# Kernel optimization log

Hardware: AMD Instinct MI355X
Metric: run time of the kernel (lower is better)

Reference implementation:

```python
import jax, jax.numpy as jnp
import numpy as np

B, NT, NC, NN = 2, 64, 1024, 1024
C, H = 1024, 16
HD = C // H
N = NT + NC + NN
EPS = 1e-5
NEG = -1e30


def _ln(t, w, b):
    # LayerNorm over last dim (head_dim), torch eps=1e-5
    mu = jnp.mean(t, axis=-1, keepdims=True)
    var = jnp.mean(jnp.square(t - mu), axis=-1, keepdims=True)
    return (t - mu) * jax.lax.rsqrt(var + EPS) * w + b


def _rope(q, k, pos):
    # q,k: [B,H,S,HD]; pos: [B,S]; rotate-half RoPE, base 10000
    hd = q.shape[-1]
    half = hd // 2
    inv_freq = 1.0 / (10000.0 ** (jnp.arange(half, dtype=jnp.float32) / half))
    ang = pos.astype(jnp.float32)[:, None, :, None] * inv_freq  # [B,1,S,half]
    cos, sin = jnp.cos(ang), jnp.sin(ang)
    def rot(t):
        t1, t2 = t[..., :half], t[..., half:]
        return jnp.concatenate([t1 * cos - t2 * sin, t2 * cos + t1 * sin], axis=-1)
    return rot(q), rot(k)


def setup_inputs() -> dict:
    key = jax.random.key(0)
    ks = jax.random.split(key, 4)
    s = 0.02
    return {
        "x": jax.random.normal(ks[0], (B, N, C), jnp.float32),
        "position_ids": jnp.broadcast_to(jnp.arange(NC + NN, dtype=jnp.int32), (B, NC + NN)),
        "text_position_ids": jnp.broadcast_to(jnp.arange(NT, dtype=jnp.int32), (B, NT)),
        "attention_mask": jnp.tril(jnp.ones((N, N), dtype=bool)),
        "n_text": NT, "n_clean": NC, "n_noised": NN,
        "qkv_w": jax.random.normal(ks[1], (3, 3 * C, C), jnp.float32) * s,
        "qkv_b": jnp.zeros((3, 3 * C), jnp.float32),
        "qn_w": jnp.ones((3, HD), jnp.float32),
        "qn_b": jnp.zeros((3, HD), jnp.float32),
        "kn_w": jnp.ones((3, HD), jnp.float32),
        "kn_b": jnp.zeros((3, HD), jnp.float32),
        "proj_w": jax.random.normal(ks[2], (3, C, C), jnp.float32) * s,
        "proj_b": jnp.zeros((3, C), jnp.float32),
    }


def reference(x, position_ids, text_position_ids, attention_mask, n_text, n_clean, n_noised,
              qkv_w, qkv_b, qn_w, qn_b, kn_w, kn_b, proj_w, proj_b):
    Bx, Nx, Cx = x.shape
    hd = qn_w.shape[-1]
    nh = Cx // hd
    b0, b1 = n_text, n_text + n_clean
    segs = (x[:, :b0], x[:, b0:b1], x[:, b1:])  # text / clean / noised

    qs, kks, vvs = [], [], []
    for i, xs in enumerate(segs):
        S = xs.shape[1]
        qkv = jnp.einsum('bsc,oc->bso', xs, qkv_w[i]) + qkv_b[i]
        qkv = qkv.reshape(Bx, S, 3, nh, hd).transpose(2, 0, 3, 1, 4)  # [3,B,H,S,hd]
        q = _ln(qkv[0], qn_w[i], qn_b[i])
        k = _ln(qkv[1], kn_w[i], kn_b[i])
        qs.append(q); kks.append(k); vvs.append(qkv[2])

    img_q = jnp.concatenate([qs[1], qs[2]], axis=2)
    img_k = jnp.concatenate([kks[1], kks[2]], axis=2)
    img_q, img_k = _rope(img_q, img_k, position_ids)
    txt_q, txt_k = _rope(qs[0], kks[0], text_position_ids)

    q = jnp.concatenate([txt_q, img_q], axis=2)
    k = jnp.concatenate([txt_k, img_k], axis=2)
    v = jnp.concatenate(vvs, axis=2)

    scale = 1.0 / np.sqrt(hd).astype(np.float32)
    scores = jnp.einsum('bhqd,bhkd->bhqk', q, k) * scale
    scores = jnp.where(attention_mask, scores, NEG)
    attn = jax.nn.softmax(scores, axis=-1)
    out = jnp.einsum('bhqk,bhkd->bhqd', attn, v)
    out = out.transpose(0, 2, 1, 3).reshape(Bx, Nx, Cx)

    o_segs = (out[:, :b0], out[:, b0:b1], out[:, b1:])
    outs = [jnp.einsum('bsc,oc->bso', o_segs[i], proj_w[i]) + proj_b[i] for i in range(3)]
    return jnp.concatenate(outs, axis=1)
```

## Files before the change

kernel.cpp:

```cpp
#include <hip/hip_runtime.h>
#include <hip/hip_bf16.h>

#define BB   2
#define NT   64
#define NC   1024
#define NN   1024
#define NTOK (NT + NC + NN)
#define CC   1024
#define HH   16
#define HD   64
#define K3   (3 * CC)
#define EPSV 1e-5f

typedef __attribute__((ext_vector_type(8))) short short8;
typedef __attribute__((ext_vector_type(4))) float f32x4;

__device__ __forceinline__ short bf16raw(float x) {
    __hip_bfloat16 h = __float2bfloat16(x);
    return *(short*)&h;
}

#define GL_LDS(gptr, lptr) \
    __builtin_amdgcn_global_load_lds( \
        (const __attribute__((address_space(1))) void*)(gptr), \
        (__attribute__((address_space(3))) void*)(lptr), 16, 0, 0)

__global__ __launch_bounds__(256) void cast_bf16(const float* __restrict__ src,
                                                 __hip_bfloat16* __restrict__ dst, int n) {
    int i = blockIdx.x * 256 + threadIdx.x;
    int stride = gridDim.x * 256;
    for (; i < n; i += stride) dst[i] = __float2bfloat16(src[i]);
}

__global__ __launch_bounds__(256) void gemm_qkv(
    const __hip_bfloat16* __restrict__ A,
    const __hip_bfloat16* __restrict__ Wb,
    const float* __restrict__ biasb,
    const int* __restrict__ pos_ids,
    const int* __restrict__ tpos_ids,
    const float* __restrict__ qn_w, const float* __restrict__ qn_b,
    const float* __restrict__ kn_w, const float* __restrict__ kn_b,
    __hip_bfloat16* __restrict__ Q,
    __hip_bfloat16* __restrict__ Kg,
    __hip_bfloat16* __restrict__ Vt)
{
    __shared__ short buf[128 * 134];
    short* As = buf;
    short* Bs = buf + 4096;

    int tid = threadIdx.x;
    int lane = tid & 63, w = tid >> 6;
    int l15 = lane & 15, quad = lane >> 4;
    int wm = w >> 1, wn = w & 1;

    int y = blockIdx.y;
    int seg, tm;
    if (y < 16)      { seg = 1; tm = y * 128; }
    else if (y < 32) { seg = 2; tm = (y - 16) * 128; }
    else             { seg = 0; tm = 0; }
    int S = (seg == 0) ? 64 : 1024;
    int seg_start = (seg == 0) ? 0 : (seg == 1 ? NT : NT + NC);
    const short* W = (const short*)Wb + (size_t)seg * K3 * CC;
    const float* bias = biasb + (size_t)seg * K3;
    int tileN = blockIdx.x * 128;

    const short* aptr[2];
    const short* bptr[2];
#pragma unroll
    for (int j = 0; j < 2; ++j) {
        int c = j * 256 + tid;
        int row = c >> 2, u = c & 3;
        int ar = tm + row;
        int arow = (ar / S) * NTOK + seg_start + (ar % S);
        aptr[j] = (const short*)A + (size_t)arow * CC + u * 8;
        bptr[j] = W + (size_t)(tileN + row) * CC + u * 8;
    }

    f32x4 zero = {0.f, 0.f, 0.f, 0.f};
    f32x4 acc[4][4];
#pragma unroll
    for (int mb = 0; mb < 4; ++mb)
#pragma unroll
        for (int nb = 0; nb < 4; ++nb) acc[mb][nb] = zero;

    for (int k0 = 0; k0 < CC; k0 += 32) {
        __syncthreads();
#pragma unroll
        for (int j = 0; j < 2; ++j) {
            int c8 = (j * 256 + tid) * 8;
            GL_LDS(aptr[j] + k0, As + c8);
            GL_LDS(bptr[j] + k0, Bs + c8);
        }
        __syncthreads();

        short8 af[4], bf[4];
#pragma unroll
        for (int mb = 0; mb < 4; ++mb)
            af[mb] = *(const short8*)&As[((wm * 64 + mb * 16 + l15) * 4 + quad) * 8];
#pragma unroll
        for (int nb = 0; nb < 4; ++nb)
            bf[nb] = *(const short8*)&Bs[((wn * 64 + nb * 16 + l15) * 4 + quad) * 8];
#pragma unroll
        for (int mb = 0; mb < 4; ++mb)
#pragma unroll
            for (int nb = 0; nb < 4; ++nb)
                acc[mb][nb] = __builtin_amdgcn_mfma_f32_16x16x32_bf16(af[mb], bf[nb], acc[mb][nb], 0, 0, 0);
    }

    int sect = tileN >> 10;
    int head = ((tileN & 1023) >> 6) + wn;

    if (sect < 2) {
        const float* nw = (sect == 0 ? qn_w : kn_w) + seg * HD;
        const float* nbv = (sect == 0 ? qn_b : kn_b) + seg * HD;
        float lw[4], lb[4], bcol[4];
#pragma unroll
        for (int nb = 0; nb < 4; ++nb) {
            lw[nb] = nw[nb * 16 + l15];
            lb[nb] = nbv[nb * 16 + l15];
            bcol[nb] = bias[tileN + wn * 64 + nb * 16 + l15];
        }
        float invf0 = expf(-9.210340371976184f * (float)l15 * (1.0f / 32.0f));
        float invf1 = expf(-9.210340371976184f * (float)(16 + l15) * (1.0f / 32.0f));
        __hip_bfloat16* dst = (sect == 0) ? Q : Kg;
        float qscale = (sect == 0) ? 0.125f : 1.0f;

#pragma unroll
        for (int mb = 0; mb < 4; ++mb) {
#pragma unroll
            for (int r = 0; r < 4; ++r) {
                int ar = tm + wm * 64 + mb * 16 + quad * 4 + r;
                int bb = ar / S;
                int nloc = seg_start + (ar % S);
                float v[4];
#pragma unroll
                for (int nb = 0; nb < 4; ++nb) v[nb] = acc[mb][nb][r] + bcol[nb];

                float mu = v[0] + v[1] + v[2] + v[3];
#pragma unroll
                for (int off = 8; off >= 1; off >>= 1) mu += __shfl_xor(mu, off);
                mu *= (1.0f / 64.0f);
                float t[4];
                float var = 0.f;
#pragma unroll
                for (int nb = 0; nb < 4; ++nb) { t[nb] = v[nb] - mu; var += t[nb] * t[nb]; }
#pragma unroll
                for (int off = 8; off >= 1; off >>= 1) var += __shfl_xor(var, off);
                var *= (1.0f / 64.0f);
                float rstd = rsqrtf(var + EPSV);
#pragma unroll
                for (int nb = 0; nb < 4; ++nb) v[nb] = t[nb] * rstd * lw[nb] + lb[nb];

                int pos = (seg == 0) ? tpos_ids[bb * NT + nloc]
                                     : pos_ids[bb * (NC + NN) + (nloc - NT)];
                float s0, c0, s1, c1;
                sincosf((float)pos * invf0, &s0, &c0);
                sincosf((float)pos * invf1, &s1, &c1);
                float o0 = (v[0] * c0 - v[2] * s0) * qscale;
                float o1 = (v[1] * c1 - v[3] * s1) * qscale;
                float o2 = (v[2] * c0 + v[0] * s0) * qscale;
                float o3 = (v[3] * c1 + v[1] * s1) * qscale;

                short* dp = (short*)dst + ((size_t)(bb * HH + head) * NTOK + nloc) * HD;
                dp[0 * 16 + l15] = bf16raw(o0);
                dp[1 * 16 + l15] = bf16raw(o1);
                dp[2 * 16 + l15] = bf16raw(o2);
                dp[3 * 16 + l15] = bf16raw(o3);
            }
        }
    } else {
        __syncthreads();
        float bcol[4];
#pragma unroll
        for (int nb = 0; nb < 4; ++nb) bcol[nb] = bias[tileN + wn * 64 + nb * 16 + l15];
#pragma unroll
        for (int mb = 0; mb < 4; ++mb) {
#pragma unroll
            for (int r = 0; r < 4; ++r) {
                int tok = wm * 64 + mb * 16 + quad * 4 + r;
#pragma unroll
                for (int nb = 0; nb < 4; ++nb) {
                    int col = wn * 64 + nb * 16 + l15;
                    buf[col * 134 + tok] = bf16raw(acc[mb][nb][r] + bcol[nb]);
                }
            }
        }
        __syncthreads();
#pragma unroll
        for (int it = 0; it < 8; ++it) {
            int idx = it * 256 + tid;
            int row = idx >> 4;
            int tc = (idx & 15) * 8;
            int vcol = (tileN - 2048) + row;
            int h = vcol >> 6, d = vcol & 63;
            int ar = tm + tc;
            int bb = ar / S;
            int nloc = seg_start + (ar % S);
            short8 val = *(const short8*)&buf[row * 134 + tc];
            *(short8*)((short*)Vt + ((size_t)(bb * HH + h) * HD + d) * NTOK + nloc) = val;
        }
    }
}

__global__ __launch_bounds__(256) void gemm128(
    const __hip_bfloat16* __restrict__ A,
    const __hip_bfloat16* __restrict__ Wb,
    const float* __restrict__ biasb,
    float* __restrict__ Cout,
    int Kdim, int Nout)
{
    __shared__ short As[128 * 32];
    __shared__ short Bs[128 * 32];

    int tid = threadIdx.x;
    int lane = tid & 63, w = tid >> 6;
    int l15 = lane & 15, quad = lane >> 4;
    int wm = w >> 1, wn = w & 1;

    int y = blockIdx.y;
    int seg, tm;
    if (y < 16)      { seg = 1; tm = y * 128; }
    else if (y < 32) { seg = 2; tm = (y - 16) * 128; }
    else             { seg = 0; tm = 0; }
    int S = (seg == 0) ? 64 : 1024;
    int seg_start = (seg == 0) ? 0 : (seg == 1 ? NT : NT + NC);
    const short* W = (const short*)Wb + (size_t)seg * Nout * Kdim;
    const float* bias = biasb + (size_t)seg * Nout;
    int tileN = blockIdx.x * 128;

    const short* aptr[2];
    const short* bptr[2];
#pragma unroll
    for (int j = 0; j < 2; ++j) {
        int c = j * 256 + tid;
        int row = c >> 2, u = c & 3;
        int ar = tm + row;
        int arow = (ar / S) * NTOK + seg_start + (ar % S);
        aptr[j] = (const short*)A + (size_t)arow * Kdim + u * 8;
        bptr[j] = W + (size_t)(tileN + row) * Kdim + u * 8;
    }

    f32x4 zero = {0.f, 0.f, 0.f, 0.f};
    f32x4 acc[4][4];
#pragma unroll
    for (int mb = 0; mb < 4; ++mb)
#pragma unroll
        for (int nb = 0; nb < 4; ++nb) acc[mb][nb] = zero;

    for (int k0 = 0; k0 < Kdim; k0 += 32) {
        __syncthreads();
#pragma unroll
        for (int j = 0; j < 2; ++j) {
            int c8 = (j * 256 + tid) * 8;
            GL_LDS(aptr[j] + k0, As + c8);
            GL_LDS(bptr[j] + k0, Bs + c8);
        }
        __syncthreads();

        short8 af[4], bf[4];
#pragma unroll
        for (int mb = 0; mb < 4; ++mb)
            af[mb] = *(const short8*)&As[((wm * 64 + mb * 16 + l15) * 4 + quad) * 8];
#pragma unroll
        for (int nb = 0; nb < 4; ++nb)
            bf[nb] = *(const short8*)&Bs[((wn * 64 + nb * 16 + l15) * 4 + quad) * 8];
#pragma unroll
        for (int mb = 0; mb < 4; ++mb)
#pragma unroll
            for (int nb = 0; nb < 4; ++nb)
                acc[mb][nb] = __builtin_amdgcn_mfma_f32_16x16x32_bf16(af[mb], bf[nb], acc[mb][nb], 0, 0, 0);
    }

#pragma unroll
    for (int mb = 0; mb < 4; ++mb) {
#pragma unroll
        for (int r = 0; r < 4; ++r) {
            int ar = tm + wm * 64 + mb * 16 + quad * 4 + r;
            int crow = (ar / S) * NTOK + seg_start + (ar % S);
            float* cp = Cout + (size_t)crow * Nout + tileN;
#pragma unroll
            for (int nb = 0; nb < 4; ++nb) {
                int col = wn * 64 + nb * 16 + l15;
                cp[col] = acc[mb][nb][r] + bias[tileN + col];
            }
        }
    }
}

__global__ __launch_bounds__(256) void attn_mfma(
    const __hip_bfloat16* __restrict__ Q,
    const __hip_bfloat16* __restrict__ Kg,
    const __hip_bfloat16* __restrict__ Vt,
    __hip_bfloat16* __restrict__ O)
{
    __shared__ short Ks[64][72];
    __shared__ short Vs[64][72];
    __shared__ short Ps[4][16][72];

    int tid = threadIdx.x;
    int lane = tid & 63, w = tid >> 6;
    int quad = lane >> 4, l15 = lane & 15;
    int bh = blockIdx.y, b = bh >> 4, h = bh & 15;
    int q0 = (gridDim.x - 1 - blockIdx.x) * 64;
    size_t base = (size_t)bh * NTOK * HD;

    int qrow = q0 + w * 16 + l15;
    short8 qf0 = *(const short8*)((const short*)Q + base + (size_t)qrow * HD + quad * 8);
    short8 qf1 = *(const short8*)((const short*)Q + base + (size_t)qrow * HD + 32 + quad * 8);

    f32x4 zero = {0.f, 0.f, 0.f, 0.f};
    f32x4 oacc[4] = {zero, zero, zero, zero};
    float l[4] = {0.f, 0.f, 0.f, 0.f};

    int ntiles = q0 / 64 + 1;

    for (int t = 0; t < ntiles; ++t) {
        __syncthreads();
        for (int i = tid; i < 512; i += 256) {
            int r = i >> 3, c = (i & 7) * 8;
            *(short8*)&Ks[r][c] = *(const short8*)((const short*)Kg + base + (size_t)(t * 64 + r) * HD + c);
            *(short8*)&Vs[r][c] = *(const short8*)((const short*)Vt + base + (size_t)r * NTOK + t * 64 + c);
        }
        __syncthreads();

        f32x4 s[4];
#pragma unroll
        for (int kb = 0; kb < 4; ++kb) {
            short8 kf0 = *(const short8*)&Ks[kb * 16 + l15][quad * 8];
            short8 kf1 = *(const short8*)&Ks[kb * 16 + l15][32 + quad * 8];
            f32x4 z = zero;
            z = __builtin_amdgcn_mfma_f32_16x16x32_bf16(qf0, kf0, z, 0, 0, 0);
            z = __builtin_amdgcn_mfma_f32_16x16x32_bf16(qf1, kf1, z, 0, 0, 0);
            s[kb] = z;
        }

#pragma unroll
        for (int r = 0; r < 4; ++r) {
            int qg = q0 + w * 16 + quad * 4 + r;
#pragma unroll
            for (int kb = 0; kb < 4; ++kb) {
                int kgk = t * 64 + kb * 16 + l15;
                float p = (kgk <= qg) ? __expf(s[kb][r]) : 0.f;
                Ps[w][quad * 4 + r][kb * 16 + l15] = bf16raw(p);
                l[r] += p;
            }
        }

        __builtin_amdgcn_wave_barrier();

#pragma unroll
        for (int sl = 0; sl < 2; ++sl) {
            short8 pf = *(const short8*)&Ps[w][l15][sl * 32 + quad * 8];
#pragma unroll
            for (int db = 0; db < 4; ++db) {
                short8 vf = *(const short8*)&Vs[db * 16 + l15][sl * 32 + quad * 8];
                oacc[db] = __builtin_amdgcn_mfma_f32_16x16x32_bf16(pf, vf, oacc[db], 0, 0, 0);
            }
        }
    }

#pragma unroll
    for (int r = 0; r < 4; ++r) {
#pragma unroll
        for (int off = 8; off >= 1; off >>= 1) l[r] += __shfl_xor(l[r], off);
    }

#pragma unroll
    for (int r = 0; r < 4; ++r) {
        int qg = q0 + w * 16 + quad * 4 + r;
        float inv_l = 1.0f / l[r];
#pragma unroll
        for (int db = 0; db < 4; ++db) {
            O[(size_t)(b * NTOK + qg) * CC + h * HD + db * 16 + l15] =
                __float2bfloat16(oacc[db][r] * inv_l);
        }
    }
}

extern "C" void kernel_launch(void* const* d_in, const int* in_sizes, int n_in,
                              void* d_out, int out_size, void* d_ws, size_t ws_size,
                              hipStream_t stream) {
    const float* x      = (const float*)d_in[0];
    const int* pos_ids  = (const int*)d_in[1];
    const int* tpos_ids = (const int*)d_in[2];
    const float* qkv_w  = (const float*)d_in[7];
    const float* qkv_b  = (const float*)d_in[8];
    const float* qn_w   = (const float*)d_in[9];
    const float* qn_b   = (const float*)d_in[10];
    const float* kn_w   = (const float*)d_in[11];
    const float* kn_b   = (const float*)d_in[12];
    const float* proj_w = (const float*)d_in[13];
    const float* proj_b = (const float*)d_in[14];
    float* out = (float*)d_out;

    const size_t n_x    = (size_t)BB * NTOK * CC;
    const size_t n_qkvw = (size_t)3 * K3 * CC;
    const size_t n_prjw = (size_t)3 * CC * CC;

    __hip_bfloat16* x_bf    = (__hip_bfloat16*)d_ws;
    __hip_bfloat16* qkvw_bf = x_bf + n_x;
    __hip_bfloat16* prjw_bf = qkvw_bf + n_qkvw;
    __hip_bfloat16* Qbf  = prjw_bf + n_prjw;
    __hip_bfloat16* Kbf  = Qbf + n_x;
    __hip_bfloat16* Vtbf = Kbf + n_x;
    __hip_bfloat16* attn_bf = x_bf;

    cast_bf16<<<(int)((n_x + 255) / 256), 256, 0, stream>>>(x, x_bf, (int)n_x);
    cast_bf16<<<(int)((n_qkvw + 255) / 256), 256, 0, stream>>>(qkv_w, qkvw_bf, (int)n_qkvw);
    cast_bf16<<<(int)((n_prjw + 255) / 256), 256, 0, stream>>>(proj_w, prjw_bf, (int)n_prjw);

    gemm_qkv<<<dim3(K3 / 128, 33), 256, 0, stream>>>(
        x_bf, qkvw_bf, qkv_b, pos_ids, tpos_ids,
        qn_w, qn_b, kn_w, kn_b, Qbf, Kbf, Vtbf);

    attn_mfma<<<dim3(NTOK / 64, BB * HH), 256, 0, stream>>>(Qbf, Kbf, Vtbf, attn_bf);

    gemm128<<<dim3(CC / 128, 33), 256, 0, stream>>>(
        attn_bf, prjw_bf, proj_b, out, CC, CC);
}
```

Before: 319.8 us.

## Fuse casts, widen GEMM K-tiles with XOR swizzle, coalesce QK stores, enlarge attention tiles

Merges the three fp32-to-bf16 cast launches into one vectorized kernel. The QKV and projection GEMMs now use BK=64 tiles with an XOR-swizzled LDS layout to cut bank conflicts and halve the barrier count. Q/K epilogue outputs are staged through LDS so global writes become 16-byte rows. The projection GEMM moves to 64-row M tiles, doubling the block count for better occupancy. Attention loads 128-key tiles, and a wave skips compute when the whole tile lies past its causal limit, at the cost of extra LDS per block.

```diff
diff --git a/kernel.cpp b/kernel.cpp
--- a/kernel.cpp
+++ b/kernel.cpp
@@ -14,6 +14,7 @@
 
 typedef __attribute__((ext_vector_type(8))) short short8;
 typedef __attribute__((ext_vector_type(4))) float f32x4;
+typedef __attribute__((ext_vector_type(4))) float float4v;
 
 __device__ __forceinline__ short bf16raw(float x) {
     __hip_bfloat16 h = __float2bfloat16(x);
@@ -25,11 +26,24 @@
         (const __attribute__((address_space(1))) void*)(gptr), \
         (__attribute__((address_space(3))) void*)(lptr), 16, 0, 0)
 
-__global__ __launch_bounds__(256) void cast_bf16(const float* __restrict__ src,
-                                                 __hip_bfloat16* __restrict__ dst, int n) {
+__global__ __launch_bounds__(256) void cast_all(
+    const float* __restrict__ s0, const float* __restrict__ s1, const float* __restrict__ s2,
+    __hip_bfloat16* __restrict__ d0, __hip_bfloat16* __restrict__ d1, __hip_bfloat16* __restrict__ d2,
+    int n0, int n1, int n2)
+{
     int i = blockIdx.x * 256 + threadIdx.x;
     int stride = gridDim.x * 256;
-    for (; i < n; i += stride) dst[i] = __float2bfloat16(src[i]);
+    int ntot = n0 + n1 + n2;
+    for (; i < ntot; i += stride) {
+        const float* sp; short* dp; int j;
+        if (i < n0)            { sp = s0; dp = (short*)d0; j = i; }
+        else if (i < n0 + n1)  { sp = s1; dp = (short*)d1; j = i - n0; }
+        else                   { sp = s2; dp = (short*)d2; j = i - n0 - n1; }
+        float4v v = *(const float4v*)(sp + (size_t)j * 4);
+        short4 o;
+        o.x = bf16raw(v.x); o.y = bf16raw(v.y); o.z = bf16raw(v.z); o.w = bf16raw(v.w);
+        *(short4*)(dp + (size_t)j * 4) = o;
+    }
 }
 
 __global__ __launch_bounds__(256) void gemm_qkv(
@@ -46,12 +60,13 @@
 {
     __shared__ short buf[128 * 134];
     short* As = buf;
-    short* Bs = buf + 4096;
+    short* Bs = buf + 8192;
 
     int tid = threadIdx.x;
     int lane = tid & 63, w = tid >> 6;
     int l15 = lane & 15, quad = lane >> 4;
     int wm = w >> 1, wn = w & 1;
+    int r7 = l15 & 7;
 
     int y = blockIdx.y;
     int seg, tm;
@@ -64,12 +79,12 @@
     const float* bias = biasb + (size_t)seg * K3;
     int tileN = blockIdx.x * 128;
 
-    const short* aptr[2];
-    const short* bptr[2];
-#pragma unroll
-    for (int j = 0; j < 2; ++j) {
+    const short* aptr[4];
+    const short* bptr[4];
+#pragma unroll
+    for (int j = 0; j < 4; ++j) {
         int c = j * 256 + tid;
-        int row = c >> 2, u = c & 3;
+        int row = c >> 3, u = (c & 7) ^ (row & 7);
         int ar = tm + row;
         int arow = (ar / S) * NTOK + seg_start + (ar % S);
         aptr[j] = (const short*)A + (size_t)arow * CC + u * 8;
@@ -83,32 +98,36 @@
 #pragma unroll
         for (int nb = 0; nb < 4; ++nb) acc[mb][nb] = zero;
 
-    for (int k0 = 0; k0 < CC; k0 += 32) {
-        __syncthreads();
-#pragma unroll
-        for (int j = 0; j < 2; ++j) {
+    for (int k0 = 0; k0 < CC; k0 += 64) {
+        __syncthreads();
+#pragma unroll
+        for (int j = 0; j < 4; ++j) {
             int c8 = (j * 256 + tid) * 8;
             GL_LDS(aptr[j] + k0, As + c8);
             GL_LDS(bptr[j] + k0, Bs + c8);
         }
         __syncthreads();
 
-        short8 af[4], bf[4];
-#pragma unroll
-        for (int mb = 0; mb < 4; ++mb)
-            af[mb] = *(const short8*)&As[((wm * 64 + mb * 16 + l15) * 4 + quad) * 8];
-#pragma unroll
-        for (int nb = 0; nb < 4; ++nb)
-            bf[nb] = *(const short8*)&Bs[((wn * 64 + nb * 16 + l15) * 4 + quad) * 8];
-#pragma unroll
-        for (int mb = 0; mb < 4; ++mb)
+#pragma unroll
+        for (int s = 0; s < 2; ++s) {
+            int sx = ((s * 4 + quad) ^ r7) * 8;
+            short8 af[4], bf[4];
+#pragma unroll
+            for (int mb = 0; mb < 4; ++mb)
+                af[mb] = *(const short8*)&As[(wm * 64 + mb * 16 + l15) * 64 + sx];
 #pragma unroll
             for (int nb = 0; nb < 4; ++nb)
-                acc[mb][nb] = __builtin_amdgcn_mfma_f32_16x16x32_bf16(af[mb], bf[nb], acc[mb][nb], 0, 0, 0);
+                bf[nb] = *(const short8*)&Bs[(wn * 64 + nb * 16 + l15) * 64 + sx];
+#pragma unroll
+            for (int mb = 0; mb < 4; ++mb)
+#pragma unroll
+                for (int nb = 0; nb < 4; ++nb)
+                    acc[mb][nb] = __builtin_amdgcn_mfma_f32_16x16x32_bf16(af[mb], bf[nb], acc[mb][nb], 0, 0, 0);
+        }
     }
 
     int sect = tileN >> 10;
-    int head = ((tileN & 1023) >> 6) + wn;
+    __syncthreads();
 
     if (sect < 2) {
         const float* nw = (sect == 0 ? qn_w : kn_w) + seg * HD;
@@ -122,14 +141,14 @@
         }
         float invf0 = expf(-9.210340371976184f * (float)l15 * (1.0f / 32.0f));
         float invf1 = expf(-9.210340371976184f * (float)(16 + l15) * (1.0f / 32.0f));
-        __hip_bfloat16* dst = (sect == 0) ? Q : Kg;
         float qscale = (sect == 0) ? 0.125f : 1.0f;
 
 #pragma unroll
         for (int mb = 0; mb < 4; ++mb) {
 #pragma unroll
             for (int r = 0; r < 4; ++r) {
-                int ar = tm + wm * 64 + mb * 16 + quad * 4 + r;
+                int tok = wm * 64 + mb * 16 + quad * 4 + r;
+                int ar = tm + tok;
                 int bb = ar / S;
                 int nloc = seg_start + (ar % S);
                 float v[4];
@@ -156,20 +175,28 @@
                 float s0, c0, s1, c1;
                 sincosf((float)pos * invf0, &s0, &c0);
                 sincosf((float)pos * invf1, &s1, &c1);
-                float o0 = (v[0] * c0 - v[2] * s0) * qscale;
-                float o1 = (v[1] * c1 - v[3] * s1) * qscale;
-                float o2 = (v[2] * c0 + v[0] * s0) * qscale;
-                float o3 = (v[3] * c1 + v[1] * s1) * qscale;
-
-                short* dp = (short*)dst + ((size_t)(bb * HH + head) * NTOK + nloc) * HD;
-                dp[0 * 16 + l15] = bf16raw(o0);
-                dp[1 * 16 + l15] = bf16raw(o1);
-                dp[2 * 16 + l15] = bf16raw(o2);
-                dp[3 * 16 + l15] = bf16raw(o3);
-            }
+                short* bp = &buf[tok * 134 + wn * 64];
+                bp[0 * 16 + l15] = bf16raw((v[0] * c0 - v[2] * s0) * qscale);
+                bp[1 * 16 + l15] = bf16raw((v[1] * c1 - v[3] * s1) * qscale);
+                bp[2 * 16 + l15] = bf16raw((v[2] * c0 + v[0] * s0) * qscale);
+                bp[3 * 16 + l15] = bf16raw((v[3] * c1 + v[1] * s1) * qscale);
+            }
+        }
+        __syncthreads();
+        __hip_bfloat16* dst = (sect == 0) ? Q : Kg;
+        int head_base = (tileN & 1023) >> 6;
+#pragma unroll
+        for (int it = 0; it < 8; ++it) {
+            int idx = it * 256 + tid;
+            int tok = idx >> 4, cc = (idx & 15) * 8;
+            int ar = tm + tok;
+            int bb = ar / S;
+            int nloc = seg_start + (ar % S);
+            int hh2 = head_base + (cc >> 6), d = cc & 63;
+            *(short8*)((short*)dst + ((size_t)(bb * HH + hh2) * NTOK + nloc) * HD + d) =
+                *(const short8*)&buf[tok * 134 + cc];
         }
     } else {
-        __syncthreads();
         float bcol[4];
 #pragma unroll
         for (int nb = 0; nb < 4; ++nb) bcol[nb] = bias[tileN + wn * 64 + nb * 16 + l15];
@@ -202,82 +229,91 @@
     }
 }
 
-__global__ __launch_bounds__(256) void gemm128(
+__global__ __launch_bounds__(256) void gemm_proj(
     const __hip_bfloat16* __restrict__ A,
     const __hip_bfloat16* __restrict__ Wb,
     const float* __restrict__ biasb,
-    float* __restrict__ Cout,
-    int Kdim, int Nout)
+    float* __restrict__ Cout)
 {
-    __shared__ short As[128 * 32];
-    __shared__ short Bs[128 * 32];
+    __shared__ short As[64 * 64];
+    __shared__ short Bs[128 * 64];
 
     int tid = threadIdx.x;
     int lane = tid & 63, w = tid >> 6;
     int l15 = lane & 15, quad = lane >> 4;
     int wm = w >> 1, wn = w & 1;
+    int r7 = l15 & 7;
 
     int y = blockIdx.y;
     int seg, tm;
-    if (y < 16)      { seg = 1; tm = y * 128; }
-    else if (y < 32) { seg = 2; tm = (y - 16) * 128; }
-    else             { seg = 0; tm = 0; }
+    if (y < 32)      { seg = 1; tm = y * 64; }
+    else if (y < 64) { seg = 2; tm = (y - 32) * 64; }
+    else             { seg = 0; tm = (y - 64) * 64; }
     int S = (seg == 0) ? 64 : 1024;
     int seg_start = (seg == 0) ? 0 : (seg == 1 ? NT : NT + NC);
-    const short* W = (const short*)Wb + (size_t)seg * Nout * Kdim;
-    const float* bias = biasb + (size_t)seg * Nout;
+    const short* W = (const short*)Wb + (size_t)seg * CC * CC;
+    const float* bias = biasb + (size_t)seg * CC;
     int tileN = blockIdx.x * 128;
 
     const short* aptr[2];
-    const short* bptr[2];
+    const short* bptr[4];
 #pragma unroll
     for (int j = 0; j < 2; ++j) {
         int c = j * 256 + tid;
-        int row = c >> 2, u = c & 3;
+        int row = c >> 3, u = (c & 7) ^ (row & 7);
         int ar = tm + row;
         int arow = (ar / S) * NTOK + seg_start + (ar % S);
-        aptr[j] = (const short*)A + (size_t)arow * Kdim + u * 8;
-        bptr[j] = W + (size_t)(tileN + row) * Kdim + u * 8;
+        aptr[j] = (const short*)A + (size_t)arow * CC + u * 8;
+    }
+#pragma unroll
+    for (int j = 0; j < 4; ++j) {
+        int c = j * 256 + tid;
+        int row = c >> 3, u = (c & 7) ^ (row & 7);
+        bptr[j] = W + (size_t)(tileN + row) * CC + u * 8;
     }
 
     f32x4 zero = {0.f, 0.f, 0.f, 0.f};
-    f32x4 acc[4][4];
-#pragma unroll
-    for (int mb = 0; mb < 4; ++mb)
+    f32x4 acc[2][4];
+#pragma unroll
+    for (int mb = 0; mb < 2; ++mb)
 #pragma unroll
         for (int nb = 0; nb < 4; ++nb) acc[mb][nb] = zero;
 
-    for (int k0 = 0; k0 < Kdim; k0 += 32) {
-        __syncthreads();
-#pragma unroll
-        for (int j = 0; j < 2; ++j) {
-            int c8 = (j * 256 + tid) * 8;
-            GL_LDS(aptr[j] + k0, As + c8);
-            GL_LDS(bptr[j] + k0, Bs + c8);
-        }
-        __syncthreads();
-
-        short8 af[4], bf[4];
-#pragma unroll
-        for (int mb = 0; mb < 4; ++mb)
-            af[mb] = *(const short8*)&As[((wm * 64 + mb * 16 + l15) * 4 + quad) * 8];
-#pragma unroll
-        for (int nb = 0; nb < 4; ++nb)
-            bf[nb] = *(const short8*)&Bs[((wn * 64 + nb * 16 + l15) * 4 + quad) * 8];
-#pragma unroll
-        for (int mb = 0; mb < 4; ++mb)
+    for (int k0 = 0; k0 < CC; k0 += 64) {
+        __syncthreads();
+#pragma unroll
+        for (int j = 0; j < 2; ++j)
+            GL_LDS(aptr[j] + k0, As + (j * 256 + tid) * 8);
+#pragma unroll
+        for (int j = 0; j < 4; ++j)
+            GL_LDS(bptr[j] + k0, Bs + (j * 256 + tid) * 8);
+        __syncthreads();
+
+#pragma unroll
+        for (int s = 0; s < 2; ++s) {
+            int sx = ((s * 4 + quad) ^ r7) * 8;
+            short8 af[2], bf[4];
+#pragma unroll
+            for (int mb = 0; mb < 2; ++mb)
+                af[mb] = *(const short8*)&As[(wm * 32 + mb * 16 + l15) * 64 + sx];
 #pragma unroll
             for (int nb = 0; nb < 4; ++nb)
-                acc[mb][nb] = __builtin_amdgcn_mfma_f32_16x16x32_bf16(af[mb], bf[nb], acc[mb][nb], 0, 0, 0);
-    }
-
-#pragma unroll
-    for (int mb = 0; mb < 4; ++mb) {
+                bf[nb] = *(const short8*)&Bs[(wn * 64 + nb * 16 + l15) * 64 + sx];
+#pragma unroll
+            for (int mb = 0; mb < 2; ++mb)
+#pragma unroll
+                for (int nb = 0; nb < 4; ++nb)
+                    acc[mb][nb] = __builtin_amdgcn_mfma_f32_16x16x32_bf16(af[mb], bf[nb], acc[mb][nb], 0, 0, 0);
+        }
+    }
+
+#pragma unroll
+    for (int mb = 0; mb < 2; ++mb) {
 #pragma unroll
         for (int r = 0; r < 4; ++r) {
-            int ar = tm + wm * 64 + mb * 16 + quad * 4 + r;
+            int ar = tm + wm * 32 + mb * 16 + quad * 4 + r;
             int crow = (ar / S) * NTOK + seg_start + (ar % S);
-            float* cp = Cout + (size_t)crow * Nout + tileN;
+            float* cp = Cout + (size_t)crow * CC + tileN;
 #pragma unroll
             for (int nb = 0; nb < 4; ++nb) {
                 int col = wn * 64 + nb * 16 + l15;
@@ -293,9 +329,9 @@
     const __hip_bfloat16* __restrict__ Vt,
     __hip_bfloat16* __restrict__ O)
 {
-    __shared__ short Ks[64][72];
-    __shared__ short Vs[64][72];
-    __shared__ short Ps[4][16][72];
+    __shared__ short Ks[128][72];
+    __shared__ short Vs[64][136];
+    __shared__ short Ps[4][16][136];
 
     int tid = threadIdx.x;
     int lane = tid & 63, w = tid >> 6;
@@ -312,44 +348,58 @@
     f32x4 oacc[4] = {zero, zero, zero, zero};
     float l[4] = {0.f, 0.f, 0.f, 0.f};
 
-    int ntiles = q0 / 64 + 1;
+    int qmax_w = q0 + w * 16 + 15;
+    int ntiles = (q0 + 191) >> 7;
 
     for (int t = 0; t < ntiles; ++t) {
         __syncthreads();
-        for (int i = tid; i < 512; i += 256) {
-            int r = i >> 3, c = (i & 7) * 8;
-            *(short8*)&Ks[r][c] = *(const short8*)((const short*)Kg + base + (size_t)(t * 64 + r) * HD + c);
-            *(short8*)&Vs[r][c] = *(const short8*)((const short*)Vt + base + (size_t)r * NTOK + t * 64 + c);
-        }
-        __syncthreads();
-
-        f32x4 s[4];
-#pragma unroll
-        for (int kb = 0; kb < 4; ++kb) {
-            short8 kf0 = *(const short8*)&Ks[kb * 16 + l15][quad * 8];
-            short8 kf1 = *(const short8*)&Ks[kb * 16 + l15][32 + quad * 8];
-            f32x4 z = zero;
-            z = __builtin_amdgcn_mfma_f32_16x16x32_bf16(qf0, kf0, z, 0, 0, 0);
-            z = __builtin_amdgcn_mfma_f32_16x16x32_bf16(qf1, kf1, z, 0, 0, 0);
-            s[kb] = z;
-        }
-
-#pragma unroll
-        for (int r = 0; r < 4; ++r) {
-            int qg = q0 + w * 16 + quad * 4 + r;
-#pragma unroll
-            for (int kb = 0; kb < 4; ++kb) {
-                int kgk = t * 64 + kb * 16 + l15;
-                float p = (kgk <= qg) ? __expf(s[kb][r]) : 0.f;
-                Ps[w][quad * 4 + r][kb * 16 + l15] = bf16raw(p);
-                l[r] += p;
+        for (int i = tid; i < 2048; i += 256) {
+            if (i < 1024) {
+                int kr = i >> 3, kc = (i & 7) * 8;
+                int row = t * 128 + kr;
+                if (row >= NTOK) row = NTOK - 1;
+                *(short8*)&Ks[kr][kc] = *(const short8*)((const short*)Kg + base + (size_t)row * HD + kc);
+            } else {
+                int j = i - 1024;
+                int vr = j >> 4, vc = (j & 15) * 8;
+                int col = t * 128 + vc;
+                if (col + 8 > NTOK) col = NTOK - 8;
+                *(short8*)&Vs[vr][vc] = *(const short8*)((const short*)Vt + base + (size_t)vr * NTOK + col);
+            }
+        }
+        __syncthreads();
+        if (t * 128 > qmax_w) continue;
+
+#pragma unroll
+        for (int half = 0; half < 2; ++half) {
+            f32x4 s[4];
+#pragma unroll
+            for (int kb4 = 0; kb4 < 4; ++kb4) {
+                int kb = half * 4 + kb4;
+                short8 kf0 = *(const short8*)&Ks[kb * 16 + l15][quad * 8];
+                short8 kf1 = *(const short8*)&Ks[kb * 16 + l15][32 + quad * 8];
+                f32x4 z = zero;
+                z = __builtin_amdgcn_mfma_f32_16x16x32_bf16(qf0, kf0, z, 0, 0, 0);
+                z = __builtin_amdgcn_mfma_f32_16x16x32_bf16(qf1, kf1, z, 0, 0, 0);
+                s[kb4] = z;
+            }
+#pragma unroll
+            for (int r = 0; r < 4; ++r) {
+                int qg = q0 + w * 16 + quad * 4 + r;
+#pragma unroll
+                for (int kb4 = 0; kb4 < 4; ++kb4) {
+                    int kgk = t * 128 + (half * 4 + kb4) * 16 + l15;
+                    float p = (kgk <= qg) ? __expf(s[kb4][r]) : 0.f;
+                    Ps[w][quad * 4 + r][(half * 4 + kb4) * 16 + l15] = bf16raw(p);
+                    l[r] += p;
+                }
             }
         }
 
         __builtin_amdgcn_wave_barrier();
 
 #pragma unroll
-        for (int sl = 0; sl < 2; ++sl) {
+        for (int sl = 0; sl < 4; ++sl) {
             short8 pf = *(const short8*)&Ps[w][l15][sl * 32 + quad * 8];
 #pragma unroll
             for (int db = 0; db < 4; ++db) {
@@ -405,9 +455,8 @@
     __hip_bfloat16* Vtbf = Kbf + n_x;
     __hip_bfloat16* attn_bf = x_bf;
 
-    cast_bf16<<<(int)((n_x + 255) / 256), 256, 0, stream>>>(x, x_bf, (int)n_x);
-    cast_bf16<<<(int)((n_qkvw + 255) / 256), 256, 0, stream>>>(qkv_w, qkvw_bf, (int)n_qkvw);
-    cast_bf16<<<(int)((n_prjw + 255) / 256), 256, 0, stream>>>(proj_w, prjw_bf, (int)n_prjw);
+    cast_all<<<1024, 256, 0, stream>>>(x, qkv_w, proj_w, x_bf, qkvw_bf, prjw_bf,
+                                       (int)(n_x / 4), (int)(n_qkvw / 4), (int)(n_prjw / 4));
 
     gemm_qkv<<<dim3(K3 / 128, 33), 256, 0, stream>>>(
         x_bf, qkvw_bf, qkv_b, pos_ids, tpos_ids,
@@ -415,6 +464,5 @@
 
     attn_mfma<<<dim3(NTOK / 64, BB * HH), 256, 0, stream>>>(Qbf, Kbf, Vtbf, attn_bf);
 
-    gemm128<<<dim3(CC / 128, 33), 256, 0, stream>>>(
-        attn_bf, prjw_bf, proj_b, out, CC, CC);
-}
+    gemm_proj<<<dim3(CC / 128, 66), 256, 0, stream>>>(attn_bf, prjw_bf, proj_b, out);
+}
```

Measured after the change: 320.9 us. No clear change (+0.3%).
